# Performance work log

Measured on AMD Instinct MI355X. Metric: run time of the kernel, lower is better.

Reference implementation:

```python
import jax, jax.numpy as jnp
import numpy as np

LN_EPS = 1e-5

def _layer_norm(x, w, b):
    mu = jnp.mean(x, axis=-1, keepdims=True)
    var = jnp.mean(jnp.square(x - mu), axis=-1, keepdims=True)
    return (x - mu) * jax.lax.rsqrt(var + LN_EPS) * w + b

def setup_inputs() -> dict:
    key = jax.random.key(0)
    ks = jax.random.split(key, 8)
    B, NODES, D = 32, 202, 64
    return {
        "embeddings": jax.random.normal(ks[0], (B, NODES, D), dtype=jnp.float32),
        "ln_w": jnp.ones((D,), jnp.float32),
        "ln_b": jnp.zeros((D,), jnp.float32),
        "W1_w": jax.random.normal(ks[1], (D, D), jnp.float32) * 0.05,
        "W1_b": jax.random.normal(ks[2], (D,), jnp.float32) * 0.05,
        "W2_w": jax.random.normal(ks[3], (D, D), jnp.float32) * 0.05,
        "W2_b": jax.random.normal(ks[4], (D,), jnp.float32) * 0.05,
        "a1_w": jax.random.normal(ks[5], (3 * D,), jnp.float32) * 0.05,
        "a1_b": jax.random.normal(ks[6], (1,), jnp.float32) * 0.05,
        "a2_w": jax.random.normal(ks[7], (3 * D,), jnp.float32) * 0.05,
        "a2_b": jax.random.normal(jax.random.fold_in(key, 99), (1,), jnp.float32) * 0.05,
    }

def reference(embeddings, ln_w, ln_b, W1_w, W1_b, W2_w, W2_b, a1_w, a1_b, a2_w, a2_b):
    # embeddings: [B, 2+N, D]; dropout p=0 (eval) -> identity
    emb = _layer_norm(embeddings, ln_w, ln_b)
    uid0 = emb[:, 0, :]          # [B, D]
    iid0 = emb[:, 1, :]          # [B, D]
    iatt = emb[:, 2:, :]         # [B, N, D]
    ua = uid0[:, None, :] * iatt  # [B, N, D]
    # value[b,i,j,:] = LN(ua[b,i] * ua[b,j])  -- the big [B,N,N,D] tensor
    value = _layer_norm(ua[:, :, None, :] * ua[:, None, :, :], ln_w, ln_b)

    def head(Ww, Wb, aw, ab):
        # Linear W applied to expanded query/key/iid collapses to per-row projections;
        # a([wq; wk; wiid]) decomposes additively across the three concat blocks.
        wua = ua @ Ww.T + Wb                  # [B, N, D]  (shared by query rows and key cols)
        wiid = iid0 @ Ww.T + Wb               # [B, D]
        aq, ak, ai = jnp.split(aw, 3)
        sq = wua @ aq                         # [B, N]  query contribution (index i)
        sk = wua @ ak                         # [B, N]  key contribution (index j)
        si = wiid @ ai                        # [B]
        scores = sq[:, :, None] + sk[:, None, :] + si[:, None, None] + ab[0]  # [B,N,N]
        scores = jax.nn.leaky_relu(scores)    # negative_slope=0.01 (torch default)
        alphas = jax.nn.softmax(scores, axis=-1)
        # original sums over dim=-2 (index i), softmax was over j -- kept faithfully
        return jnp.einsum('bij,bijd->bjd', alphas, value)  # [B, N, D]

    att1 = head(W1_w, W1_b, a1_w, a1_b)
    att2 = head(W2_w, W2_b, a2_w, a2_b)
    att_value = (att1 + att2) * 0.5           # [B, N, D]
    ui = (uid0 * iid0)[:, None, :]            # [B, 1, D]
    em_out = jnp.concatenate([ui, att_value], axis=1)  # [B, N+1, D]
    return jax.nn.leaky_relu(em_out)
```

## Files before the change

kernel.cpp:

```cpp
#include <hip/hip_runtime.h>
#include <hip/hip_bf16.h>

#define LN_EPS 1e-5f
#define BB 32
#define NI 200
#define NIP 208
#define DD 64

typedef __attribute__((ext_vector_type(8))) short bf16x8;
typedef __attribute__((ext_vector_type(4))) short bf16x4;
typedef __attribute__((ext_vector_type(4))) float f32x4;

__device__ __forceinline__ float leaky(float x) { return fmaxf(x, 0.01f * x); }
__device__ __forceinline__ short f2bf(float x) {
  __hip_bfloat16 h = __float2bfloat16(x);
  return *reinterpret_cast<short*>(&h);
}
__device__ __forceinline__ float bf2fs(short s) {
  unsigned u = ((unsigned)(unsigned short)s) << 16;
  return __uint_as_float(u);
}
__device__ __forceinline__ bf16x8 sq8(bf16x8 a) {
  bf16x8 r;
#pragma unroll
  for (int k = 0; k < 8; k++) { float f = bf2fs(a[k]); r[k] = f2bf(f * f); }
  return r;
}

#define WS_SC 0
#define WS_T  (WS_SC + BB*NIP*4)
#define WS_CR (WS_T + BB*2)
#define WS_UB (WS_CR + 8)

__device__ __forceinline__ void reduce2(float& a, float& b) {
#pragma unroll
  for (int m = 1; m < 64; m <<= 1) { a += __shfl_xor(a, m, 64); b += __shfl_xor(b, m, 64); }
}
__device__ __forceinline__ void reduce4(float& a, float& b, float& c, float& d) {
#pragma unroll
  for (int m = 1; m < 64; m <<= 1) {
    a += __shfl_xor(a, m, 64); b += __shfl_xor(b, m, 64);
    c += __shfl_xor(c, m, 64); d += __shfl_xor(d, m, 64);
  }
}
__device__ __forceinline__ float reduce1(float a) {
#pragma unroll
  for (int m = 1; m < 64; m <<= 1) a += __shfl_xor(a, m, 64);
  return a;
}
__device__ __forceinline__ void rmax2(float& a, float& b) {
#pragma unroll
  for (int m = 1; m < 64; m <<= 1) {
    a = fmaxf(a, __shfl_xor(a, m, 64));
    b = fmaxf(b, __shfl_xor(b, m, 64));
  }
}

__global__ void __launch_bounds__(256) gat_kX(const float* __restrict__ emb,
                                              const float* __restrict__ lw,
                                              const float* __restrict__ lb,
                                              const float* __restrict__ W1,
                                              const float* __restrict__ W1b,
                                              const float* __restrict__ W2,
                                              const float* __restrict__ W2b,
                                              const float* __restrict__ a1,
                                              const float* __restrict__ a2,
                                              float* __restrict__ ws,
                                              float* __restrict__ out) {
  int b = blockIdx.y, tid = threadIdx.x, wv = tid >> 6, lane = tid & 63;
  int node = blockIdx.x * 4 + wv;
  __shared__ float v_sh[4][64];
  __shared__ float vi_sh[2][64];
  __shared__ float iid_sh[64];

  float w = lw[lane], bi = lb[lane];
  auto lnrow = [&](int n) -> float {
    float x = emb[(size_t)(b * 202 + n) * 64 + lane];
    float s = x, s2 = x * x;
    reduce2(s, s2);
    float mu = s * (1.f / 64);
    float var = fmaxf(s2 * (1.f / 64) - mu * mu, 0.f);
    return (x - mu) * rsqrtf(var + LN_EPS) * w + bi;
  };
  float u = lnrow(0);
  float y = 0.f;
  if (node >= 1 && node <= 201) y = lnrow(node);
  if (node == 1) {
    iid_sh[lane] = y;
    out[(size_t)(b * 201) * 64 + lane] = leaky(u * y);
  }
  if (wv == 0) {
    float p0 = 0, p1 = 0;
#pragma unroll 8
    for (int d = 0; d < 64; d++) {
      float x = W1[d * 64 + lane];
      p0 = fmaf(x, a1[d], p0); p1 = fmaf(x, a1[64 + d], p1);
    }
    v_sh[0][lane] = p0; v_sh[1][lane] = p1;
  } else if (wv == 1) {
    float p0 = 0, p1 = 0;
#pragma unroll 8
    for (int d = 0; d < 64; d++) {
      float x = W2[d * 64 + lane];
      p0 = fmaf(x, a2[d], p0); p1 = fmaf(x, a2[64 + d], p1);
    }
    v_sh[2][lane] = p0; v_sh[3][lane] = p1;
  } else if (blockIdx.x == 0 && wv == 2) {
    float p = 0;
#pragma unroll 8
    for (int d = 0; d < 64; d++) p = fmaf(W1[d * 64 + lane], a1[128 + d], p);
    vi_sh[0][lane] = p;
  } else if (blockIdx.x == 0 && wv == 3) {
    float p = 0;
#pragma unroll 8
    for (int d = 0; d < 64; d++) p = fmaf(W2[d * 64 + lane], a2[128 + d], p);
    vi_sh[1][lane] = p;
  }
  __syncthreads();

  if (node >= 2 && node <= 201) {
    int i = node - 2;
    float a = u * y;
    ((unsigned short*)(ws + WS_UB))[(size_t)(b * NI + i) * 64 + lane] =
        (unsigned short)f2bf(a);
    float p0 = a * v_sh[0][lane], p1 = a * v_sh[1][lane];
    float p2 = a * v_sh[2][lane], p3 = a * v_sh[3][lane];
    reduce4(p0, p1, p2, p3);
    if (lane == 0) {
      f32x4 sc = {p0, p1, p2, p3};
      *(f32x4*)(ws + WS_SC + (size_t)(b * NIP + i) * 4) = sc;
    }
  }
  if (blockIdx.x == 0 && wv == 0) {
    float q0 = iid_sh[lane] * vi_sh[0][lane];
    float q1 = iid_sh[lane] * vi_sh[1][lane];
    reduce2(q0, q1);
    if (lane == 0) { ws[WS_T + b * 2] = q0; ws[WS_T + b * 2 + 1] = q1; }
  }
  if (blockIdx.x == 0 && b == 0 && wv == 1) {
    float c0 = reduce1(W1b[lane] * a1[lane]);
    float c1 = reduce1(W1b[lane] * a1[64 + lane]);
    float c2 = reduce1(W1b[lane] * a1[128 + lane]);
    float c3 = reduce1(W2b[lane] * a2[lane]);
    float c4 = reduce1(W2b[lane] * a2[64 + lane]);
    float c5 = reduce1(W2b[lane] * a2[128 + lane]);
    if (lane == 0) {
      ws[WS_CR + 0] = c0; ws[WS_CR + 1] = c1; ws[WS_CR + 2] = c2;
      ws[WS_CR + 3] = c3; ws[WS_CR + 4] = c4; ws[WS_CR + 5] = c5;
    }
  }
}

#define SM_UA   0
#define SM_UAT  26624
#define SM_G0   55296
#define SM_G1   62464
#define SM_PART 69632
#define SM_ST   70656
#define SM_SKV  75648
#define SM_WMX  77312

__global__ void __launch_bounds__(512) gat_kY(const float* __restrict__ ws,
                                              const float* __restrict__ lw,
                                              const float* __restrict__ lb,
                                              const float* __restrict__ a1b,
                                              const float* __restrict__ a2b,
                                              float* __restrict__ out) {
  __shared__ __align__(16) char smem[77376];
  int b = blockIdx.y, bx = blockIdx.x, tid = threadIdx.x;
  int wv = tid >> 6, lane = tid & 63, q = lane >> 4, col = lane & 15;
  int half = wv >> 2, wq = wv & 3;

  short* sUA  = (short*)(smem + SM_UA);
  short* sUAT = (short*)(smem + SM_UAT);
  short* sG0  = (short*)(smem + SM_G0);
  short* sG1  = (short*)(smem + SM_G1);
  float* sPart = (float*)(smem + SM_PART);
  float* sST   = (float*)(smem + SM_ST);
  float* skv   = (float*)(smem + SM_SKV);
  float* wmx   = (float*)(smem + SM_WMX);

  const unsigned short* uwb =
      (const unsigned short*)(ws + WS_UB) + (size_t)b * NI * 64;

  for (int idx = tid; idx < 1664; idx += 512) {
    int itile = idx >> 7, rem = idx & 127, kh = rem >> 6, ln = rem & 63;
    int node = itile * 16 + (ln & 15);
    int dbase = kh * 32 + (ln >> 4) * 8;
    bf16x8 pk;
    if (node < NI) pk = *(const bf16x8*)(uwb + node * 64 + dbase);
    else {
#pragma unroll
      for (int k = 0; k < 8; k++) pk[k] = 0;
    }
    *(bf16x8*)(sUA + idx * 8) = pk;
  }
  {
    int d = tid & 63, ir = (tid >> 6) & 3, ph = tid >> 8;
    for (int p = ph; p < 7; p += 2) {
      int i0 = p * 32 + ir * 8;
      bf16x8 pk;
#pragma unroll
      for (int u = 0; u < 8; u++)
        pk[u] = (i0 + u < NI) ? (short)uwb[(i0 + u) * 64 + d] : (short)0;
      int off = ((p * 4 + (d >> 4)) * 64 + ((d & 15) + 16 * ir)) * 8;
      *(bf16x8*)(sUAT + off) = pk;
    }
  }
  if (tid < 128) ((int*)sG0)[1664 + tid] = 0;
  else if (tid < 256) ((int*)sG1)[1664 + (tid - 128)] = 0;

  float c0 = ws[WS_CR + 0], c1 = ws[WS_CR + 1], c2 = ws[WS_CR + 2];
  float c3 = ws[WS_CR + 3], c4 = ws[WS_CR + 4], c5 = ws[WS_CR + 5];
  float t1 = ws[WS_T + b * 2] + c2 + a1b[0];
  float t2 = ws[WS_T + b * 2 + 1] + c5 + a2b[0];
  if (tid < NIP) {
    f32x4 sc = *(const f32x4*)(ws + WS_SC + (size_t)(b * NIP + tid) * 4);
    float* st = sST + tid * 6;
    if (tid < NI) {
      st[0] = sc.x + c0 + t1;
      st[3] = sc.z + c3 + t2;
    } else { st[0] = 0; st[3] = 0; }
    st[1] = 0; st[2] = 0; st[4] = 0; st[5] = 0;
    skv[0 * NIP + tid] = sc.y + c1;
    skv[1 * NIP + tid] = sc.w + c4;
  }
  __syncthreads();

  float m1 = (tid < NI) ? skv[0 * NIP + tid] : -3e38f;
  float m2 = (tid < NI) ? skv[1 * NIP + tid] : -3e38f;
  rmax2(m1, m2);
  if (lane == 0) { wmx[wv * 2] = m1; wmx[wv * 2 + 1] = m2; }
  __syncthreads();

  {
    int sh = -1, si = 0;
    if (tid < NI) { sh = 0; si = tid; }
    else if (tid >= 256 && tid < 256 + NI) { sh = 1; si = tid - 256; }
    if (sh >= 0) {
      float mx = -3e38f;
#pragma unroll
      for (int k = 0; k < 8; k++) mx = fmaxf(mx, wmx[k * 2 + sh]);
      float* st = sST + si * 6;
      float base = st[sh * 3];
      float rm = leaky(base + mx);
      const float* skh = skv + sh * NIP;
      float den = 0.f;
#pragma unroll 4
      for (int j = 0; j < NI; j++) {
        float s = base + skh[j];
        den += __expf(fmaxf(s, 0.01f * s) - rm);
      }
      st[sh * 3 + 1] = rm;
      st[sh * 3 + 2] = 1.0f / den;
    }
  }
  __syncthreads();

  int jt = bx * 2 + half;
  bool act = (jt < 13);
  short* sGh = half ? sG1 : sG0;
  float* sPh = sPart + half * 128;
  float skj1 = 0, skj2 = 0;
  bf16x8 bf0, bf1, b2f0, b2f1;
  if (act) {
    bf0 = *(bf16x8*)(sUA + ((jt * 2 + 0) * 64 + lane) * 8);
    bf1 = *(bf16x8*)(sUA + ((jt * 2 + 1) * 64 + lane) * 8);
    b2f0 = sq8(bf0); b2f1 = sq8(bf1);
    int jglob = jt * 16 + col;
    skj1 = skv[0 * NIP + jglob]; skj2 = skv[1 * NIP + jglob];
    float mpart = 0.f, spart = 0.f;
    for (int it = wq; it < 13; it += 4) {
      bf16x8 af0 = *(bf16x8*)(sUA + ((it * 2 + 0) * 64 + lane) * 8);
      bf16x8 af1 = *(bf16x8*)(sUA + ((it * 2 + 1) * 64 + lane) * 8);
      bf16x8 a2f0 = sq8(af0), a2f1 = sq8(af1);
      f32x4 s = {0, 0, 0, 0}, t = {0, 0, 0, 0};
      s = __builtin_amdgcn_mfma_f32_16x16x32_bf16(af0, bf0, s, 0, 0, 0);
      s = __builtin_amdgcn_mfma_f32_16x16x32_bf16(af1, bf1, s, 0, 0, 0);
      t = __builtin_amdgcn_mfma_f32_16x16x32_bf16(a2f0, b2f0, t, 0, 0, 0);
      t = __builtin_amdgcn_mfma_f32_16x16x32_bf16(a2f1, b2f1, t, 0, 0, 0);
      bf16x4 gp;
#pragma unroll
      for (int r = 0; r < 4; r++) {
        int i = it * 16 + q * 4 + r;
        const float* st = sST + i * 6;
        float mu = s[r] * (1.f / 64);
        float var = fmaxf(t[r] * (1.f / 64) - mu * mu, 0.f);
        float inv = rsqrtf(var + LN_EPS);
        float sc1 = st[0] + skj1;
        float e1 = __expf(fmaxf(sc1, 0.01f * sc1) - st[1]) * st[2];
        float sc2 = st[3] + skj2;
        float e2 = __expf(fmaxf(sc2, 0.01f * sc2) - st[4]) * st[5];
        float c = 0.5f * (e1 + e2);
        float g = c * inv;
        mpart = fmaf(g, mu, mpart);
        spart += c;
        gp[r] = f2bf(g);
      }
      int kl = (it & 1) * 16 + q * 4;
      int off = ((it >> 1) * 64 + (col + 16 * (kl >> 3))) * 8 + (kl & 7);
      *(bf16x4*)(sGh + off) = gp;
    }
    mpart += __shfl_xor(mpart, 16, 64); mpart += __shfl_xor(mpart, 32, 64);
    spart += __shfl_xor(spart, 16, 64); spart += __shfl_xor(spart, 32, 64);
    if (lane < 16) {
      sPh[(wq * 2 + 0) * 16 + lane] = mpart;
      sPh[(wq * 2 + 1) * 16 + lane] = spart;
    }
  }
  __syncthreads();

  if (act) {
    f32x4 acc = {0, 0, 0, 0};
#pragma unroll
    for (int kt = 0; kt < 7; kt++) {
      bf16x8 ga = *(bf16x8*)(sGh + (kt * 64 + lane) * 8);
      bf16x8 ub = *(bf16x8*)(sUAT + ((kt * 4 + wq) * 64 + lane) * 8);
      acc = __builtin_amdgcn_mfma_f32_16x16x32_bf16(ga, ub, acc, 0, 0, 0);
    }
    int d = wq * 16 + col;
    float w = lw[d], bia = lb[d];
#pragma unroll
    for (int r = 0; r < 4; r++) {
      int jl = q * 4 + r, jg = jt * 16 + jl;
      if (jg < NI) {
        float m = sPh[0 * 16 + jl] + sPh[2 * 16 + jl] +
                  sPh[4 * 16 + jl] + sPh[6 * 16 + jl];
        float S = sPh[1 * 16 + jl] + sPh[3 * 16 + jl] +
                  sPh[5 * 16 + jl] + sPh[7 * 16 + jl];
        int cn = jt * 128 + (d >> 5) * 64 + ((d >> 3) & 3) * 16 + (jg & 15);
        float uajd = bf2fs(sUA[cn * 8 + (d & 7)]);
        float att = w * (uajd * acc[r] - m) + bia * S;
        out[(size_t)(b * 201 + 1 + jg) * 64 + d] = leaky(att);
      }
    }
  }
}

extern "C" void kernel_launch(void* const* d_in, const int* in_sizes, int n_in,
                              void* d_out, int out_size, void* d_ws, size_t ws_size,
                              hipStream_t stream) {
  const float* emb = (const float*)d_in[0];
  const float* lw  = (const float*)d_in[1];
  const float* lb  = (const float*)d_in[2];
  const float* W1  = (const float*)d_in[3];
  const float* W1b = (const float*)d_in[4];
  const float* W2  = (const float*)d_in[5];
  const float* W2b = (const float*)d_in[6];
  const float* a1  = (const float*)d_in[7];
  const float* a1b = (const float*)d_in[8];
  const float* a2  = (const float*)d_in[9];
  const float* a2b = (const float*)d_in[10];
  float* ws = (float*)d_ws;
  float* out = (float*)d_out;

  gat_kX<<<dim3(51, BB), dim3(256), 0, stream>>>(emb, lw, lb, W1, W1b, W2, W2b,
                                                 a1, a2, ws, out);
  gat_kY<<<dim3(7, BB), dim3(512), 0, stream>>>(ws, lw, lb, a1b, a2b, out);
}
```

Measured before the change: 95.54 us.

## Fuse two kernels into one per-batch block, caching LN rows and squared UA in LDS

The preprocessing kernel and the attention kernel are merged into a single kernel with one 512-thread block per batch. The layer-normed rows, the score projections and the bf16 UA tiles are built directly in shared memory instead of going through a global workspace. Squared UA values are precomputed once into a separate LDS buffer rather than recomputed inside the inner loop. Each wave now handles whole j-tiles across all i-tiles and all d-tiles, which removes a block-wide sync. The cost is a much smaller grid of only 32 blocks with large LDS use, so parallelism drops sharply compared with the previous 7x32 launch.

```diff
diff --git a/kernel.cpp b/kernel.cpp
--- a/kernel.cpp
+++ b/kernel.cpp
@@ -4,7 +4,6 @@
 #define LN_EPS 1e-5f
 #define BB 32
 #define NI 200
-#define NIP 208
 #define DD 64
 
 typedef __attribute__((ext_vector_type(8))) short bf16x8;
@@ -20,17 +19,6 @@
   unsigned u = ((unsigned)(unsigned short)s) << 16;
   return __uint_as_float(u);
 }
-__device__ __forceinline__ bf16x8 sq8(bf16x8 a) {
-  bf16x8 r;
-#pragma unroll
-  for (int k = 0; k < 8; k++) { float f = bf2fs(a[k]); r[k] = f2bf(f * f); }
-  return r;
-}
-
-#define WS_SC 0
-#define WS_T  (WS_SC + BB*NIP*4)
-#define WS_CR (WS_T + BB*2)
-#define WS_UB (WS_CR + 8)
 
 __device__ __forceinline__ void reduce2(float& a, float& b) {
 #pragma unroll
@@ -56,38 +44,57 @@
   }
 }
 
-__global__ void __launch_bounds__(256) gat_kX(const float* __restrict__ emb,
-                                              const float* __restrict__ lw,
-                                              const float* __restrict__ lb,
-                                              const float* __restrict__ W1,
-                                              const float* __restrict__ W1b,
-                                              const float* __restrict__ W2,
-                                              const float* __restrict__ W2b,
-                                              const float* __restrict__ a1,
-                                              const float* __restrict__ a2,
-                                              float* __restrict__ ws,
-                                              float* __restrict__ out) {
-  int b = blockIdx.y, tid = threadIdx.x, wv = tid >> 6, lane = tid & 63;
-  int node = blockIdx.x * 4 + wv;
-  __shared__ float v_sh[4][64];
-  __shared__ float vi_sh[2][64];
-  __shared__ float iid_sh[64];
-
-  float w = lw[lane], bi = lb[lane];
-  auto lnrow = [&](int n) -> float {
-    float x = emb[(size_t)(b * 202 + n) * 64 + lane];
-    float s = x, s2 = x * x;
-    reduce2(s, s2);
-    float mu = s * (1.f / 64);
-    float var = fmaxf(s2 * (1.f / 64) - mu * mu, 0.f);
-    return (x - mu) * rsqrtf(var + LN_EPS) * w + bi;
-  };
-  float u = lnrow(0);
-  float y = 0.f;
-  if (node >= 1 && node <= 201) y = lnrow(node);
-  if (node == 1) {
-    iid_sh[lane] = y;
-    out[(size_t)(b * 201) * 64 + lane] = leaky(u * y);
+#define SM_G    0
+#define SM_UA   57344
+#define SM_UA2  83968
+#define SM_UAT  110592
+#define SM_ST   139264
+#define SM_KV   144256
+#define SM_V    145920
+#define SM_MS   147456
+#define SM_WMX  148480
+#define SM_MISC 148544
+#define SM_TOTAL 148576
+
+__global__ void __launch_bounds__(512, 1)
+gat_fused(const float* __restrict__ emb,
+          const float* __restrict__ lw,
+          const float* __restrict__ lb,
+          const float* __restrict__ W1,
+          const float* __restrict__ W1b,
+          const float* __restrict__ W2,
+          const float* __restrict__ W2b,
+          const float* __restrict__ a1,
+          const float* __restrict__ a1b,
+          const float* __restrict__ a2,
+          const float* __restrict__ a2b,
+          float* __restrict__ out) {
+  __shared__ __align__(16) char smem[SM_TOTAL];
+  float* sY   = (float*)(smem + SM_G);
+  short* sG   = (short*)(smem + SM_G);
+  short* sUA  = (short*)(smem + SM_UA);
+  short* sUA2 = (short*)(smem + SM_UA2);
+  short* sUAT = (short*)(smem + SM_UAT);
+  float* sST  = (float*)(smem + SM_ST);
+  float* sKV  = (float*)(smem + SM_KV);
+  float* sV   = (float*)(smem + SM_V);
+  float* sMS  = (float*)(smem + SM_MS);
+  float* wmx  = (float*)(smem + SM_WMX);
+  float* sMisc = (float*)(smem + SM_MISC);
+
+  int b = blockIdx.x, tid = threadIdx.x, wv = tid >> 6, lane = tid & 63;
+  int q = lane >> 4, col = lane & 15;
+
+  {
+    float w = lw[lane], bi = lb[lane];
+    for (int n = wv; n < 202; n += 8) {
+      float x = emb[(size_t)(b * 202 + n) * 64 + lane];
+      float s = x, s2 = x * x;
+      reduce2(s, s2);
+      float mu = s * (1.f / 64);
+      float var = fmaxf(s2 * (1.f / 64) - mu * mu, 0.f);
+      sY[n * 65 + lane] = (x - mu) * rsqrtf(var + LN_EPS) * w + bi;
+    }
   }
   if (wv == 0) {
     float p0 = 0, p1 = 0;
@@ -96,7 +103,7 @@
       float x = W1[d * 64 + lane];
       p0 = fmaf(x, a1[d], p0); p1 = fmaf(x, a1[64 + d], p1);
     }
-    v_sh[0][lane] = p0; v_sh[1][lane] = p1;
+    sV[0 * 64 + lane] = p0; sV[1 * 64 + lane] = p1;
   } else if (wv == 1) {
     float p0 = 0, p1 = 0;
 #pragma unroll 8
@@ -104,135 +111,102 @@
       float x = W2[d * 64 + lane];
       p0 = fmaf(x, a2[d], p0); p1 = fmaf(x, a2[64 + d], p1);
     }
-    v_sh[2][lane] = p0; v_sh[3][lane] = p1;
-  } else if (blockIdx.x == 0 && wv == 2) {
+    sV[2 * 64 + lane] = p0; sV[3 * 64 + lane] = p1;
+  } else if (wv == 2) {
     float p = 0;
 #pragma unroll 8
     for (int d = 0; d < 64; d++) p = fmaf(W1[d * 64 + lane], a1[128 + d], p);
-    vi_sh[0][lane] = p;
-  } else if (blockIdx.x == 0 && wv == 3) {
+    sV[4 * 64 + lane] = p;
+    float c0 = reduce1(W1b[lane] * a1[lane]);
+    float c1 = reduce1(W1b[lane] * a1[64 + lane]);
+    float c2 = reduce1(W1b[lane] * a1[128 + lane]);
+    if (lane == 0) { sMisc[0] = c0; sMisc[1] = c1; sMisc[2] = c2; }
+  } else if (wv == 3) {
     float p = 0;
 #pragma unroll 8
     for (int d = 0; d < 64; d++) p = fmaf(W2[d * 64 + lane], a2[128 + d], p);
-    vi_sh[1][lane] = p;
-  }
-  __syncthreads();
-
-  if (node >= 2 && node <= 201) {
-    int i = node - 2;
-    float a = u * y;
-    ((unsigned short*)(ws + WS_UB))[(size_t)(b * NI + i) * 64 + lane] =
-        (unsigned short)f2bf(a);
-    float p0 = a * v_sh[0][lane], p1 = a * v_sh[1][lane];
-    float p2 = a * v_sh[2][lane], p3 = a * v_sh[3][lane];
-    reduce4(p0, p1, p2, p3);
-    if (lane == 0) {
-      f32x4 sc = {p0, p1, p2, p3};
-      *(f32x4*)(ws + WS_SC + (size_t)(b * NIP + i) * 4) = sc;
-    }
-  }
-  if (blockIdx.x == 0 && wv == 0) {
-    float q0 = iid_sh[lane] * vi_sh[0][lane];
-    float q1 = iid_sh[lane] * vi_sh[1][lane];
-    reduce2(q0, q1);
-    if (lane == 0) { ws[WS_T + b * 2] = q0; ws[WS_T + b * 2 + 1] = q1; }
-  }
-  if (blockIdx.x == 0 && b == 0 && wv == 1) {
-    float c0 = reduce1(W1b[lane] * a1[lane]);
-    float c1 = reduce1(W1b[lane] * a1[64 + lane]);
-    float c2 = reduce1(W1b[lane] * a1[128 + lane]);
+    sV[5 * 64 + lane] = p;
     float c3 = reduce1(W2b[lane] * a2[lane]);
     float c4 = reduce1(W2b[lane] * a2[64 + lane]);
     float c5 = reduce1(W2b[lane] * a2[128 + lane]);
+    if (lane == 0) { sMisc[3] = c3; sMisc[4] = c4; sMisc[5] = c5; }
+  }
+  __syncthreads();
+
+  if (wv == 0) {
+    float u0 = sY[0 * 65 + lane];
+    float iid = sY[1 * 65 + lane];
+    out[(size_t)(b * 201) * 64 + lane] = leaky(u0 * iid);
+    float q0 = iid * sV[4 * 64 + lane], q1 = iid * sV[5 * 64 + lane];
+    reduce2(q0, q1);
     if (lane == 0) {
-      ws[WS_CR + 0] = c0; ws[WS_CR + 1] = c1; ws[WS_CR + 2] = c2;
-      ws[WS_CR + 3] = c3; ws[WS_CR + 4] = c4; ws[WS_CR + 5] = c5;
-    }
-  }
-}
-
-#define SM_UA   0
-#define SM_UAT  26624
-#define SM_G0   55296
-#define SM_G1   62464
-#define SM_PART 69632
-#define SM_ST   70656
-#define SM_SKV  75648
-#define SM_WMX  77312
-
-__global__ void __launch_bounds__(512) gat_kY(const float* __restrict__ ws,
-                                              const float* __restrict__ lw,
-                                              const float* __restrict__ lb,
-                                              const float* __restrict__ a1b,
-                                              const float* __restrict__ a2b,
-                                              float* __restrict__ out) {
-  __shared__ __align__(16) char smem[77376];
-  int b = blockIdx.y, bx = blockIdx.x, tid = threadIdx.x;
-  int wv = tid >> 6, lane = tid & 63, q = lane >> 4, col = lane & 15;
-  int half = wv >> 2, wq = wv & 3;
-
-  short* sUA  = (short*)(smem + SM_UA);
-  short* sUAT = (short*)(smem + SM_UAT);
-  short* sG0  = (short*)(smem + SM_G0);
-  short* sG1  = (short*)(smem + SM_G1);
-  float* sPart = (float*)(smem + SM_PART);
-  float* sST   = (float*)(smem + SM_ST);
-  float* skv   = (float*)(smem + SM_SKV);
-  float* wmx   = (float*)(smem + SM_WMX);
-
-  const unsigned short* uwb =
-      (const unsigned short*)(ws + WS_UB) + (size_t)b * NI * 64;
-
+      sMisc[6] = q0 + sMisc[2] + a1b[0];
+      sMisc[7] = q1 + sMisc[5] + a2b[0];
+    }
+  }
   for (int idx = tid; idx < 1664; idx += 512) {
     int itile = idx >> 7, rem = idx & 127, kh = rem >> 6, ln = rem & 63;
     int node = itile * 16 + (ln & 15);
     int dbase = kh * 32 + (ln >> 4) * 8;
-    bf16x8 pk;
-    if (node < NI) pk = *(const bf16x8*)(uwb + node * 64 + dbase);
-    else {
-#pragma unroll
-      for (int k = 0; k < 8; k++) pk[k] = 0;
+    bf16x8 pk, pk2;
+    if (node < NI) {
+      const float* yr = sY + (2 + node) * 65 + dbase;
+#pragma unroll
+      for (int k = 0; k < 8; k++) {
+        float v = sY[dbase + k] * yr[k];
+        short h = f2bf(v);
+        pk[k] = h;
+        float f = bf2fs(h);
+        pk2[k] = f2bf(f * f);
+      }
+    } else {
+#pragma unroll
+      for (int k = 0; k < 8; k++) { pk[k] = 0; pk2[k] = 0; }
     }
     *(bf16x8*)(sUA + idx * 8) = pk;
+    *(bf16x8*)(sUA2 + idx * 8) = pk2;
   }
   {
     int d = tid & 63, ir = (tid >> 6) & 3, ph = tid >> 8;
+    float ud = sY[d];
     for (int p = ph; p < 7; p += 2) {
       int i0 = p * 32 + ir * 8;
       bf16x8 pk;
 #pragma unroll
-      for (int u = 0; u < 8; u++)
-        pk[u] = (i0 + u < NI) ? (short)uwb[(i0 + u) * 64 + d] : (short)0;
+      for (int uu = 0; uu < 8; uu++) {
+        int node = i0 + uu;
+        pk[uu] = (node < NI) ? f2bf(ud * sY[(2 + node) * 65 + d]) : (short)0;
+      }
       int off = ((p * 4 + (d >> 4)) * 64 + ((d & 15) + 16 * ir)) * 8;
       *(bf16x8*)(sUAT + off) = pk;
     }
   }
-  if (tid < 128) ((int*)sG0)[1664 + tid] = 0;
-  else if (tid < 256) ((int*)sG1)[1664 + (tid - 128)] = 0;
-
-  float c0 = ws[WS_CR + 0], c1 = ws[WS_CR + 1], c2 = ws[WS_CR + 2];
-  float c3 = ws[WS_CR + 3], c4 = ws[WS_CR + 4], c5 = ws[WS_CR + 5];
-  float t1 = ws[WS_T + b * 2] + c2 + a1b[0];
-  float t2 = ws[WS_T + b * 2 + 1] + c5 + a2b[0];
-  if (tid < NIP) {
-    f32x4 sc = *(const f32x4*)(ws + WS_SC + (size_t)(b * NIP + tid) * 4);
-    float* st = sST + tid * 6;
-    if (tid < NI) {
-      st[0] = sc.x + c0 + t1;
-      st[3] = sc.z + c3 + t2;
-    } else { st[0] = 0; st[3] = 0; }
-    st[1] = 0; st[2] = 0; st[4] = 0; st[5] = 0;
-    skv[0 * NIP + tid] = sc.y + c1;
-    skv[1 * NIP + tid] = sc.w + c4;
-  }
+  {
+    float u0 = sY[lane];
+    for (int i = wv; i < NI; i += 8) {
+      float a = u0 * sY[(2 + i) * 65 + lane];
+      float p0 = a * sV[0 * 64 + lane], p1 = a * sV[1 * 64 + lane];
+      float p2 = a * sV[2 * 64 + lane], p3 = a * sV[3 * 64 + lane];
+      reduce4(p0, p1, p2, p3);
+      if (lane == 0) {
+        sST[i * 6 + 0] = p0 + sMisc[0];
+        sST[i * 6 + 3] = p2 + sMisc[3];
+        sKV[0 * 208 + i] = p1 + sMisc[1];
+        sKV[1 * 208 + i] = p3 + sMisc[4];
+      }
+    }
+  }
+  if (tid < 48) sST[1200 + tid] = 0.f;
+  if (tid < 16) sKV[(tid >> 3) * 208 + 200 + (tid & 7)] = 0.f;
   __syncthreads();
 
-  float m1 = (tid < NI) ? skv[0 * NIP + tid] : -3e38f;
-  float m2 = (tid < NI) ? skv[1 * NIP + tid] : -3e38f;
-  rmax2(m1, m2);
-  if (lane == 0) { wmx[wv * 2] = m1; wmx[wv * 2 + 1] = m2; }
+  {
+    float m1 = (tid < NI) ? sKV[tid] : -3e38f;
+    float m2 = (tid < NI) ? sKV[208 + tid] : -3e38f;
+    rmax2(m1, m2);
+    if (lane == 0) { wmx[wv * 2] = m1; wmx[wv * 2 + 1] = m2; }
+  }
   __syncthreads();
-
   {
     int sh = -1, si = 0;
     if (tid < NI) { sh = 0; si = tid; }
@@ -242,9 +216,10 @@
 #pragma unroll
       for (int k = 0; k < 8; k++) mx = fmaxf(mx, wmx[k * 2 + sh]);
       float* st = sST + si * 6;
-      float base = st[sh * 3];
+      float base = st[sh * 3] + sMisc[6 + sh];
+      st[sh * 3] = base;
       float rm = leaky(base + mx);
-      const float* skh = skv + sh * NIP;
+      const float* skh = sKV + sh * 208;
       float den = 0.f;
 #pragma unroll 4
       for (int j = 0; j < NI; j++) {
@@ -257,23 +232,29 @@
   }
   __syncthreads();
 
-  int jt = bx * 2 + half;
-  bool act = (jt < 13);
-  short* sGh = half ? sG1 : sG0;
-  float* sPh = sPart + half * 128;
-  float skj1 = 0, skj2 = 0;
-  bf16x8 bf0, bf1, b2f0, b2f1;
-  if (act) {
-    bf0 = *(bf16x8*)(sUA + ((jt * 2 + 0) * 64 + lane) * 8);
-    bf1 = *(bf16x8*)(sUA + ((jt * 2 + 1) * 64 + lane) * 8);
-    b2f0 = sq8(bf0); b2f1 = sq8(bf1);
+  short* sGw = sG + wv * 3584;
+  float* sMSw = sMS + wv * 32;
+  for (int p = 0; p < 2; p++) {
+    int jt = wv + 8 * p;
+    if (jt >= 13) break;
+    {
+      bf16x8 z;
+#pragma unroll
+      for (int k = 0; k < 8; k++) z[k] = 0;
+      if (lane >= 32) *(bf16x8*)(sGw + (6 * 64 + lane) * 8) = z;
+    }
+    bf16x8 bf0 = *(bf16x8*)(sUA + ((jt * 2 + 0) * 64 + lane) * 8);
+    bf16x8 bf1 = *(bf16x8*)(sUA + ((jt * 2 + 1) * 64 + lane) * 8);
+    bf16x8 b2f0 = *(bf16x8*)(sUA2 + ((jt * 2 + 0) * 64 + lane) * 8);
+    bf16x8 b2f1 = *(bf16x8*)(sUA2 + ((jt * 2 + 1) * 64 + lane) * 8);
     int jglob = jt * 16 + col;
-    skj1 = skv[0 * NIP + jglob]; skj2 = skv[1 * NIP + jglob];
+    float skj1 = sKV[jglob], skj2 = sKV[208 + jglob];
     float mpart = 0.f, spart = 0.f;
-    for (int it = wq; it < 13; it += 4) {
+    for (int it = 0; it < 13; it++) {
       bf16x8 af0 = *(bf16x8*)(sUA + ((it * 2 + 0) * 64 + lane) * 8);
       bf16x8 af1 = *(bf16x8*)(sUA + ((it * 2 + 1) * 64 + lane) * 8);
-      bf16x8 a2f0 = sq8(af0), a2f1 = sq8(af1);
+      bf16x8 a2f0 = *(bf16x8*)(sUA2 + ((it * 2 + 0) * 64 + lane) * 8);
+      bf16x8 a2f1 = *(bf16x8*)(sUA2 + ((it * 2 + 1) * 64 + lane) * 8);
       f32x4 s = {0, 0, 0, 0}, t = {0, 0, 0, 0};
       s = __builtin_amdgcn_mfma_f32_16x16x32_bf16(af0, bf0, s, 0, 0, 0);
       s = __builtin_amdgcn_mfma_f32_16x16x32_bf16(af1, bf1, s, 0, 0, 0);
@@ -299,39 +280,31 @@
       }
       int kl = (it & 1) * 16 + q * 4;
       int off = ((it >> 1) * 64 + (col + 16 * (kl >> 3))) * 8 + (kl & 7);
-      *(bf16x4*)(sGh + off) = gp;
+      *(bf16x4*)(sGw + off) = gp;
     }
     mpart += __shfl_xor(mpart, 16, 64); mpart += __shfl_xor(mpart, 32, 64);
     spart += __shfl_xor(spart, 16, 64); spart += __shfl_xor(spart, 32, 64);
-    if (lane < 16) {
-      sPh[(wq * 2 + 0) * 16 + lane] = mpart;
-      sPh[(wq * 2 + 1) * 16 + lane] = spart;
-    }
-  }
-  __syncthreads();
-
-  if (act) {
-    f32x4 acc = {0, 0, 0, 0};
-#pragma unroll
-    for (int kt = 0; kt < 7; kt++) {
-      bf16x8 ga = *(bf16x8*)(sGh + (kt * 64 + lane) * 8);
-      bf16x8 ub = *(bf16x8*)(sUAT + ((kt * 4 + wq) * 64 + lane) * 8);
-      acc = __builtin_amdgcn_mfma_f32_16x16x32_bf16(ga, ub, acc, 0, 0, 0);
-    }
-    int d = wq * 16 + col;
-    float w = lw[d], bia = lb[d];
-#pragma unroll
-    for (int r = 0; r < 4; r++) {
-      int jl = q * 4 + r, jg = jt * 16 + jl;
-      if (jg < NI) {
-        float m = sPh[0 * 16 + jl] + sPh[2 * 16 + jl] +
-                  sPh[4 * 16 + jl] + sPh[6 * 16 + jl];
-        float S = sPh[1 * 16 + jl] + sPh[3 * 16 + jl] +
-                  sPh[5 * 16 + jl] + sPh[7 * 16 + jl];
-        int cn = jt * 128 + (d >> 5) * 64 + ((d >> 3) & 3) * 16 + (jg & 15);
-        float uajd = bf2fs(sUA[cn * 8 + (d & 7)]);
-        float att = w * (uajd * acc[r] - m) + bia * S;
-        out[(size_t)(b * 201 + 1 + jg) * 64 + d] = leaky(att);
+    if (lane < 16) { sMSw[lane] = mpart; sMSw[16 + lane] = spart; }
+    for (int dt = 0; dt < 4; dt++) {
+      f32x4 acc = {0, 0, 0, 0};
+#pragma unroll
+      for (int kt = 0; kt < 7; kt++) {
+        bf16x8 ga = *(bf16x8*)(sGw + (kt * 64 + lane) * 8);
+        bf16x8 ub = *(bf16x8*)(sUAT + ((kt * 4 + dt) * 64 + lane) * 8);
+        acc = __builtin_amdgcn_mfma_f32_16x16x32_bf16(ga, ub, acc, 0, 0, 0);
+      }
+      int d = dt * 16 + col;
+      float wd = lw[d], bia = lb[d];
+#pragma unroll
+      for (int r = 0; r < 4; r++) {
+        int jl = q * 4 + r, jg = jt * 16 + jl;
+        if (jg < NI) {
+          float m = sMSw[jl], S = sMSw[16 + jl];
+          int cn = jt * 128 + (d >> 5) * 64 + ((d >> 3) & 3) * 16 + (jg & 15);
+          float uajd = bf2fs(sUA[cn * 8 + (d & 7)]);
+          float att = wd * (uajd * acc[r] - m) + bia * S;
+          out[(size_t)(b * 201 + 1 + jg) * 64 + d] = leaky(att);
+        }
       }
     }
   }
@@ -351,10 +324,8 @@
   const float* a1b = (const float*)d_in[8];
   const float* a2  = (const float*)d_in[9];
   const float* a2b = (const float*)d_in[10];
-  float* ws = (float*)d_ws;
   float* out = (float*)d_out;
 
-  gat_kX<<<dim3(51, BB), dim3(256), 0, stream>>>(emb, lw, lb, W1, W1b, W2, W2b,
-                                                 a1, a2, ws, out);
-  gat_kY<<<dim3(7, BB), dim3(512), 0, stream>>>(ws, lw, lb, a1b, a2b, out);
-}
+  gat_fused<<<dim3(BB), dim3(512), 0, stream>>>(emb, lw, lb, W1, W1b, W2, W2b,
+                                                a1, a1b, a2, a2b, out);
+}
```

Measured after the change: 131.5 us. 1.38x slower.
